# Kernel tuning notes

Hardware: AMD Instinct MI355X
Metric: run time of the kernel (lower is better)

## Reference

```python
import jax, jax.numpy as jnp
import numpy as np

BATCH, T, N, M = 128, 128, 128, 256


def setup_inputs() -> dict:
    key = jax.random.key(0)
    ks = jax.random.split(key, 8)
    s = lambda fan_in: 1.0 / np.sqrt(fan_in)
    return {
        "x": jax.random.normal(ks[0], (BATCH, T, N), dtype=jnp.float32),
        # attention linears (bias=False)
        "We": jax.random.uniform(ks[1], (T, 2 * M), jnp.float32, -s(2 * M), s(2 * M)),
        "Ue": jax.random.uniform(ks[2], (T, T), jnp.float32, -s(T), s(T)),
        "v_e": jax.random.uniform(ks[3], (1, T), jnp.float32, -s(T), s(T)),
        # single-layer LSTM params, PyTorch gate order (i, f, g, o)
        "W_ih": jax.random.uniform(ks[4], (4 * M, N), jnp.float32, -s(M), s(M)),
        "W_hh": jax.random.uniform(ks[5], (4 * M, M), jnp.float32, -s(M), s(M)),
        "b_ih": jax.random.uniform(ks[6], (4 * M,), jnp.float32, -s(M), s(M)),
        "b_hh": jax.random.uniform(ks[7], (4 * M,), jnp.float32, -s(M), s(M)),
    }


def reference(x, We, Ue, v_e, W_ih, W_hh, b_ih, b_hh):
    batch = x.shape[0]
    m = W_hh.shape[1]
    # Ue(x.permute(0,2,1)) is time-invariant: (b, n, T)
    Ux = jnp.einsum("btn,st->bns", x, Ue)
    bias = b_ih + b_hh
    ve = v_e[0]  # (T,)

    def step(carry, x_t):
        h, c = carry  # (b, m) each
        hs = jnp.concatenate([h, c], axis=-1)  # (b, 2m)
        # We(hs) is constant over the feature axis in the original (repeat), so broadcast
        z = jnp.tanh((hs @ We.T)[:, None, :] + Ux)  # (b, n, T)
        scores = jnp.einsum("bnt,t->bn", z, ve)  # v_e linear -> (b, n)
        alpha = jax.nn.softmax(scores, axis=1)  # softmax over features
        xw = x_t * alpha  # (b, n)
        gates = xw @ W_ih.T + h @ W_hh.T + bias  # (b, 4m)
        i, f, g, o = jnp.split(gates, 4, axis=-1)
        c2 = jax.nn.sigmoid(f) * c + jax.nn.sigmoid(i) * jnp.tanh(g)
        h2 = jax.nn.sigmoid(o) * jnp.tanh(c2)
        return (h2, c2), h2

    h0 = jnp.zeros((batch, m), dtype=x.dtype)
    c0 = jnp.zeros((batch, m), dtype=x.dtype)
    xs = jnp.transpose(x, (1, 0, 2))  # (T, b, n)
    _, outs = jax.lax.scan(step, (h0, c0), xs)
    return outs  # (T, b, m)
```

## Files before the change

kernel.cpp:

```cpp
#include <hip/hip_runtime.h>
#include <hip/hip_bf16.h>
#include <hip/hip_fp16.h>

typedef unsigned int uint32;
typedef _Float16 hf2 __attribute__((ext_vector_type(2)));

#define NT 1024

__device__ __forceinline__ float bfu(unsigned short v) { return __uint_as_float(((uint32)v) << 16); }
__device__ __forceinline__ unsigned short f2bf(float f) {
    uint32 u = __float_as_uint(f);
    u = (u + 0x7fffu + ((u >> 16) & 1u)) >> 16;
    return (unsigned short)u;
}
__device__ __forceinline__ uint32 pack_f16(float a, float b) {
    __half ha = __float2half_rn(a), hb = __float2half_rn(b);
    return (uint32)__half_as_ushort(ha) | ((uint32)__half_as_ushort(hb) << 16);
}
__device__ __forceinline__ float fexp2(float x) {
#if __has_builtin(__builtin_amdgcn_exp2f)
    return __builtin_amdgcn_exp2f(x);
#else
    return exp2f(x);
#endif
}
__device__ __forceinline__ float frcp(float x) {
#if __has_builtin(__builtin_amdgcn_rcpf)
    return __builtin_amdgcn_rcpf(x);
#else
    return __fdividef(1.f, x);
#endif
}
__device__ __forceinline__ float fast_tanh(float x) {
    float e = fexp2(x * 2.8853900817779268f);
    return fmaf(-2.f, frcp(1.f + e), 1.f);
}
__device__ __forceinline__ float fast_sigmoid(float x) {
    return frcp(1.f + fexp2(-1.4426950408889634f * x));
}
__device__ __forceinline__ float rdlane(float v, int k) {
#if __has_builtin(__builtin_amdgcn_readlane)
    return __builtin_bit_cast(float, __builtin_amdgcn_readlane(__builtin_bit_cast(int, v), k));
#else
    return __shfl(v, k);
#endif
}
__device__ __forceinline__ float fdot2(uint32 w, uint32 v, float acc) {
#if __has_builtin(__builtin_amdgcn_fdot2)
    return __builtin_amdgcn_fdot2(__builtin_bit_cast(hf2, w), __builtin_bit_cast(hf2, v), acc, false);
#else
    __half2 wh = __builtin_bit_cast(__half2, w), vh = __builtin_bit_cast(__half2, v);
    float2 wf = __half22float2(wh), vf = __half22float2(vh);
    return fmaf(wf.y, vf.y, fmaf(wf.x, vf.x, acc));
#endif
}

template <int S>
__device__ __forceinline__ void spin_ge(uint32* p, uint32 tgt) {
    if (__hip_atomic_load(p, __ATOMIC_ACQUIRE, __HIP_MEMORY_SCOPE_WORKGROUP) >= tgt) return;
    int guard = 0;
    do {
        __builtin_amdgcn_s_sleep(S);
        if (++guard > (1 << 22)) break;
    } while (__hip_atomic_load(p, __ATOMIC_ACQUIRE, __HIP_MEMORY_SCOPE_WORKGROUP) < tgt);
}
__device__ __forceinline__ void st_flag(uint32* p, uint32 v) {
    __hip_atomic_store(p, v, __ATOMIC_RELEASE, __HIP_MEMORY_SCOPE_WORKGROUP);
}
__device__ __forceinline__ void add_flag(uint32* p, uint32 v) {
    __hip_atomic_fetch_add(p, v, __ATOMIC_RELEASE, __HIP_MEMORY_SCOPE_WORKGROUP);
}

__global__ void prep_weights(const float* __restrict__ We, const float* __restrict__ W_ih,
                             const float* __restrict__ W_hh, uint32* __restrict__ We2,
                             uint32* __restrict__ Wc2) {
    int idx = blockIdx.x * 256 + threadIdx.x;
    if (idx < 32768) {
        int p = idx & 3, s = (idx >> 2) & 127, jq = idx >> 9;
        int j = 8 * jq + 2 * p;
        We2[idx] = pack_f16(We[s * 512 + j], We[s * 512 + j + 1]);
    } else if (idx < 229376) {
        int i2 = idx - 32768;
        int p = i2 & 3, q = (i2 >> 2) & 255, np = i2 >> 10;
        int g = 4 * q + p;
        int n0 = 2 * np, n1 = 2 * np + 1;
        float w0, w1;
        if (n0 < 128) {
            w0 = W_ih[g * 128 + n0];
            w1 = W_ih[g * 128 + n1];
        } else {
            w0 = W_hh[g * 256 + (n0 - 128)];
            w1 = W_hh[g * 256 + (n1 - 128)];
        }
        Wc2[i2] = pack_f16(w0, w1);
    }
}

__global__ void ux_kernel(const float* __restrict__ x, const float* __restrict__ Ue,
                          unsigned short* __restrict__ Uxg) {
    int b = blockIdx.x >> 1, h = blockIdx.x & 1;
    int n = threadIdx.x & 127, sg = threadIdx.x >> 7;
    int s0 = h * 64 + sg * 16;
    float acc[16];
#pragma unroll
    for (int k = 0; k < 16; ++k) acc[k] = 0.f;
    for (int t0 = 0; t0 < 128; t0 += 16) {
        float xv[16];
#pragma unroll
        for (int tt = 0; tt < 16; ++tt) xv[tt] = x[(b * 128 + t0 + tt) * 128 + n];
#pragma unroll
        for (int k = 0; k < 16; ++k) {
            const float4* uep = (const float4*)(Ue + (s0 + k) * 128 + t0);
            float4 u0 = uep[0], u1 = uep[1], u2 = uep[2], u3 = uep[3];
            acc[k] += xv[0] * u0.x + xv[1] * u0.y + xv[2] * u0.z + xv[3] * u0.w
                    + xv[4] * u1.x + xv[5] * u1.y + xv[6] * u1.z + xv[7] * u1.w
                    + xv[8] * u2.x + xv[9] * u2.y + xv[10] * u2.z + xv[11] * u2.w
                    + xv[12] * u3.x + xv[13] * u3.y + xv[14] * u3.z + xv[15] * u3.w;
        }
    }
#pragma unroll
    for (int k = 0; k < 16; ++k)
        Uxg[b * 16384 + (s0 + k) * 128 + n] = f2bf(acc[k]);
}

__global__ __launch_bounds__(NT, 4)
void encoder_kernel(const float* __restrict__ x, const float* __restrict__ v_e,
                    const float* __restrict__ b_ih, const float* __restrict__ b_hh,
                    const unsigned short* __restrict__ Uxg, const uint4* __restrict__ We2q,
                    const uint4* __restrict__ Wc2q, float* __restrict__ out) {
    __shared__ __align__(16) unsigned short Ux_s[16384];
    __shared__ __align__(16) uint4 We2L[6144];
    __shared__ __align__(16) float part4[6144];
    __shared__ float part1[256];
    __shared__ float part2[256];
    __shared__ __align__(16) uint32 vh_s[192];
    __shared__ __align__(16) uint32 hsh_s[256];
    __shared__ float c_s[256];
    __shared__ uint32 xw_flag, cnt1, cnt2, cnt4, cnt5;

    const int tid = threadIdx.x;
    const int b = blockIdx.x;

    {
        const uint4* src = (const uint4*)(Uxg + b * 16384);
        uint4* dst = (uint4*)Ux_s;
        for (int i = tid; i < 2048; i += NT) dst[i] = src[i];
    }
    for (int i = tid; i < 6144; i += NT) We2L[i] = We2q[i];
    if (tid < 192) vh_s[tid] = 0u;
    if (tid < 256) { hsh_s[tid] = 0u; c_s[tid] = 0.f; }
    if (tid == 0) { xw_flag = 0; cnt1 = 0; cnt2 = 0; cnt4 = 0; cnt5 = 0; }
    float bi0 = 0.f, bf0 = 0.f, bg0 = 0.f, bo0 = 0.f;
    if (tid >= 768) {
        int j = tid - 768;
        bi0 = b_ih[j] + b_hh[j];
        bf0 = b_ih[256 + j] + b_hh[256 + j];
        bg0 = b_ih[512 + j] + b_hh[512 + j];
        bo0 = b_ih[768 + j] + b_hh[768 + j];
    }
    __syncthreads();

#define NP_BLOCK(npb)                                                \
    {                                                                \
        uint4 vp4 = *(const uint4*)&vh_s[(npb)];                     \
        _Pragma("unroll")                                            \
        for (int u = 0; u < 4; ++u) {                                \
            uint32 vp = (&vp4.x)[u];                                 \
            const uint4* wp = wc + ((npb) + u) * 256;                \
            uint4 w0 = wp[0], w1 = wp[1];                            \
            a0 = fdot2(w0.x, vp, a0); a1 = fdot2(w0.y, vp, a1);      \
            a2 = fdot2(w0.z, vp, a2); a3 = fdot2(w0.w, vp, a3);      \
            a4 = fdot2(w1.x, vp, a4); a5 = fdot2(w1.y, vp, a5);      \
            a6 = fdot2(w1.z, vp, a6); a7 = fdot2(w1.w, vp, a7);      \
        }                                                            \
    }

    if (tid < 768) {
        const int ol = tid & 127, g = tid >> 7;
        if (g >= 4) __builtin_amdgcn_s_setprio(1);
        const uint4* wc = Wc2q + 2 * ol;
        for (int t = 0; t < 128; ++t) {
            float a0 = 0.f, a1 = 0.f, a2 = 0.f, a3 = 0.f;
            float a4 = 0.f, a5 = 0.f, a6 = 0.f, a7 = 0.f;
            if (g < 4) {
                spin_ge<4>(&cnt5, (uint32)(4 * t));
                const int np0 = 64 + g * 32;
#pragma unroll 2
                for (int i = 0; i < 8; ++i) NP_BLOCK(np0 + 4 * i);
            } else {
                spin_ge<1>(&cnt5, (uint32)(4 * t));
                const int s = ol, jg = g - 4;
                float acc = 0.f;
                if (jg == 0) {
#pragma unroll 4
                    for (int jq = 0; jq < 32; ++jq) {
                        uint4 w = We2L[jq * 128 + s];
                        uint4 hh = *(const uint4*)&hsh_s[4 * jq];
                        acc = fdot2(w.x, hh.x, acc);
                        acc = fdot2(w.y, hh.y, acc);
                        acc = fdot2(w.z, hh.z, acc);
                        acc = fdot2(w.w, hh.w, acc);
                    }
                } else {
#pragma unroll 4
                    for (int jq = 32; jq < 48; ++jq) {
                        uint4 w = We2L[jq * 128 + s];
                        uint4 hh = *(const uint4*)&hsh_s[4 * jq];
                        acc = fdot2(w.x, hh.x, acc);
                        acc = fdot2(w.y, hh.y, acc);
                        acc = fdot2(w.z, hh.z, acc);
                        acc = fdot2(w.w, hh.w, acc);
                    }
#pragma unroll 4
                    for (int jq = 48; jq < 64; ++jq) {
                        uint4 w = We2q[jq * 128 + s];
                        uint4 hh = *(const uint4*)&hsh_s[4 * jq];
                        acc = fdot2(w.x, hh.x, acc);
                        acc = fdot2(w.y, hh.y, acc);
                        acc = fdot2(w.z, hh.z, acc);
                        acc = fdot2(w.w, hh.w, acc);
                    }
                }
                part1[jg * 128 + s] = acc;
                if ((tid & 63) == 0) add_flag(&cnt1, 1);
                spin_ge<1>(&xw_flag, (uint32)(t + 1));
                const int np0 = jg * 32;
#pragma unroll 2
                for (int i = 0; i < 8; ++i) NP_BLOCK(np0 + 4 * i);
            }
            float4* p4 = (float4*)&part4[g * 1024 + 8 * ol];
            p4[0] = make_float4(a0, a1, a2, a3);
            p4[1] = make_float4(a4, a5, a6, a7);
            if ((tid & 63) == 0) add_flag(&cnt4, 1);
        }
    } else {
        __builtin_amdgcn_s_setprio(2);
        const int bt = tid - 768, l = tid & 63;
        const int n = bt & 127, sg = bt >> 7;
        const float ve_lane = v_e[sg * 64 + l];
        const unsigned short* uxrow = Ux_s + sg * 64 * 128 + n;
        for (int t = 0; t < 128; ++t) {
            float2 xt2;
            if (bt < 64) xt2 = *(const float2*)(x + (b * 128 + t) * 128 + 2 * l);
            spin_ge<1>(&cnt1, (uint32)(4 * (t + 1)));
            float web_lo = part1[l] + part1[128 + l];
            float web_hi = part1[64 + l] + part1[192 + l];
            float wsel = sg ? web_hi : web_lo;
            float acc0 = 0.f, acc1 = 0.f;
#pragma unroll
            for (int k = 0; k < 64; k += 2) {
                float wv0 = rdlane(wsel, k), ve0 = rdlane(ve_lane, k);
                float wv1 = rdlane(wsel, k + 1), ve1 = rdlane(ve_lane, k + 1);
                acc0 = fmaf(ve0, fast_tanh(wv0 + bfu(uxrow[k * 128])), acc0);
                acc1 = fmaf(ve1, fast_tanh(wv1 + bfu(uxrow[(k + 1) * 128])), acc1);
            }
            part2[sg * 128 + n] = acc0 + acc1;
            if (l == 0) add_flag(&cnt2, 1);
            if (bt < 64) {
                spin_ge<1>(&cnt2, (uint32)(4 * (t + 1)));
                __builtin_amdgcn_s_setprio(3);
                float v0 = part2[2 * l] + part2[128 + 2 * l];
                float v1 = part2[2 * l + 1] + part2[129 + 2 * l];
                float e0 = fexp2(v0 * 1.4426950408889634f);
                float e1 = fexp2(v1 * 1.4426950408889634f);
                float ssum = e0 + e1;
#pragma unroll
                for (int off = 32; off > 0; off >>= 1) ssum += __shfl_xor(ssum, off);
                float inv = frcp(ssum);
                vh_s[l] = pack_f16(xt2.x * e0 * inv, xt2.y * e1 * inv);
                if (bt == 0) st_flag(&xw_flag, (uint32)(t + 1));
                __builtin_amdgcn_s_setprio(2);
            }
            spin_ge<1>(&cnt4, (uint32)(12 * (t + 1)));
            const int j = bt;
            float gi = bi0, gf = bf0, gg = bg0, go = bo0;
#pragma unroll
            for (int gr = 0; gr < 6; ++gr) {
                const float* pp = part4 + gr * 1024;
                gi += pp[j]; gf += pp[256 + j];
                gg += pp[512 + j]; go += pp[768 + j];
            }
            float c = c_s[j];
            float c2 = fast_sigmoid(gf) * c + fast_sigmoid(gi) * fast_tanh(gg);
            float h2v = fast_sigmoid(go) * fast_tanh(c2);
            c_s[j] = c2;
            float hn = __shfl_xor(h2v, 1);
            float cn = __shfl_xor(c2, 1);
            if (!(j & 1)) {
                uint32 hp = pack_f16(h2v, hn);
                vh_s[64 + (j >> 1)] = hp;
                hsh_s[j >> 1] = hp;
                hsh_s[128 + (j >> 1)] = pack_f16(c2, cn);
            }
            if (l == 0) add_flag(&cnt5, 1);
            out[(t * 128 + b) * 256 + j] = h2v;
        }
    }
#undef NP_BLOCK
}

extern "C" void kernel_launch(void* const* d_in, const int* in_sizes, int n_in,
                              void* d_out, int out_size, void* d_ws, size_t ws_size,
                              hipStream_t stream) {
    const float* x    = (const float*)d_in[0];
    const float* We   = (const float*)d_in[1];
    const float* Ue   = (const float*)d_in[2];
    const float* v_e  = (const float*)d_in[3];
    const float* W_ih = (const float*)d_in[4];
    const float* W_hh = (const float*)d_in[5];
    const float* b_ih = (const float*)d_in[6];
    const float* b_hh = (const float*)d_in[7];
    float* out = (float*)d_out;

    char* w = (char*)d_ws;
    unsigned short* Uxg = (unsigned short*)w;
    uint32* We2 = (uint32*)(w + 4194304);
    uint32* Wc2 = (uint32*)(w + 4325376);

    prep_weights<<<896, 256, 0, stream>>>(We, W_ih, W_hh, We2, Wc2);
    ux_kernel<<<256, 512, 0, stream>>>(x, Ue, Uxg);
    encoder_kernel<<<128, NT, 0, stream>>>(x, v_e, b_ih, b_hh, Uxg,
                                           (const uint4*)We2, (const uint4*)Wc2, out);
}
```

Measured before the change: 1.260 ms.

## Defer softmax normalization past xw publish, busy-spin flags, rebalance We partial dot

The softmax-weighted input is published unnormalized, so the x-projection warps can start their dot products before the softmax sum reduction finishes. The reciprocal sum is written to shared memory afterwards and applied to the x-projection partial sums during the gate reduction, at the cost of one extra flag increment (the cnt4 target becomes 13 per step). Spin waits drop s_sleep in favour of pure busy polling to cut wake-up latency, which uses more issue slots while waiting. The We·hs dot product is split evenly between the two warpgroups (24 LDS chunks plus 8 global chunks each) instead of 32 versus 32.

```diff
diff --git a/kernel.cpp b/kernel.cpp
--- a/kernel.cpp
+++ b/kernel.cpp
@@ -63,6 +63,12 @@
         __builtin_amdgcn_s_sleep(S);
         if (++guard > (1 << 22)) break;
     } while (__hip_atomic_load(p, __ATOMIC_ACQUIRE, __HIP_MEMORY_SCOPE_WORKGROUP) < tgt);
+}
+__device__ __forceinline__ void spin_busy(uint32* p, uint32 tgt) {
+    int guard = 0;
+    while (__hip_atomic_load(p, __ATOMIC_ACQUIRE, __HIP_MEMORY_SCOPE_WORKGROUP) < tgt) {
+        if (++guard > (1 << 24)) break;
+    }
 }
 __device__ __forceinline__ void st_flag(uint32* p, uint32 v) {
     __hip_atomic_store(p, v, __ATOMIC_RELEASE, __HIP_MEMORY_SCOPE_WORKGROUP);
@@ -136,6 +142,7 @@
     __shared__ __align__(16) uint32 vh_s[192];
     __shared__ __align__(16) uint32 hsh_s[256];
     __shared__ float c_s[256];
+    __shared__ float inv_s;
     __shared__ uint32 xw_flag, cnt1, cnt2, cnt4, cnt5;
 
     const int tid = threadIdx.x;
@@ -149,7 +156,7 @@
     for (int i = tid; i < 6144; i += NT) We2L[i] = We2q[i];
     if (tid < 192) vh_s[tid] = 0u;
     if (tid < 256) { hsh_s[tid] = 0u; c_s[tid] = 0.f; }
-    if (tid == 0) { xw_flag = 0; cnt1 = 0; cnt2 = 0; cnt4 = 0; cnt5 = 0; }
+    if (tid == 0) { xw_flag = 0; cnt1 = 0; cnt2 = 0; cnt4 = 0; cnt5 = 0; inv_s = 0.f; }
     float bi0 = 0.f, bf0 = 0.f, bg0 = 0.f, bo0 = 0.f;
     if (tid >= 768) {
         int j = tid - 768;
@@ -188,42 +195,32 @@
 #pragma unroll 2
                 for (int i = 0; i < 8; ++i) NP_BLOCK(np0 + 4 * i);
             } else {
-                spin_ge<1>(&cnt5, (uint32)(4 * t));
+                spin_busy(&cnt5, (uint32)(4 * t));
                 const int s = ol, jg = g - 4;
+                const int lq0 = jg * 24;
+                const int gq0 = 48 + jg * 8;
                 float acc = 0.f;
-                if (jg == 0) {
+#pragma unroll
+                for (int jq = gq0; jq < gq0 + 8; ++jq) {
+                    uint4 w = We2q[jq * 128 + s];
+                    uint4 hh = *(const uint4*)&hsh_s[4 * jq];
+                    acc = fdot2(w.x, hh.x, acc);
+                    acc = fdot2(w.y, hh.y, acc);
+                    acc = fdot2(w.z, hh.z, acc);
+                    acc = fdot2(w.w, hh.w, acc);
+                }
 #pragma unroll 4
-                    for (int jq = 0; jq < 32; ++jq) {
-                        uint4 w = We2L[jq * 128 + s];
-                        uint4 hh = *(const uint4*)&hsh_s[4 * jq];
-                        acc = fdot2(w.x, hh.x, acc);
-                        acc = fdot2(w.y, hh.y, acc);
-                        acc = fdot2(w.z, hh.z, acc);
-                        acc = fdot2(w.w, hh.w, acc);
-                    }
-                } else {
-#pragma unroll 4
-                    for (int jq = 32; jq < 48; ++jq) {
-                        uint4 w = We2L[jq * 128 + s];
-                        uint4 hh = *(const uint4*)&hsh_s[4 * jq];
-                        acc = fdot2(w.x, hh.x, acc);
-                        acc = fdot2(w.y, hh.y, acc);
-                        acc = fdot2(w.z, hh.z, acc);
-                        acc = fdot2(w.w, hh.w, acc);
-                    }
-#pragma unroll 4
-                    for (int jq = 48; jq < 64; ++jq) {
-                        uint4 w = We2q[jq * 128 + s];
-                        uint4 hh = *(const uint4*)&hsh_s[4 * jq];
-                        acc = fdot2(w.x, hh.x, acc);
-                        acc = fdot2(w.y, hh.y, acc);
-                        acc = fdot2(w.z, hh.z, acc);
-                        acc = fdot2(w.w, hh.w, acc);
-                    }
+                for (int jq = lq0; jq < lq0 + 24; ++jq) {
+                    uint4 w = We2L[jq * 128 + s];
+                    uint4 hh = *(const uint4*)&hsh_s[4 * jq];
+                    acc = fdot2(w.x, hh.x, acc);
+                    acc = fdot2(w.y, hh.y, acc);
+                    acc = fdot2(w.z, hh.z, acc);
+                    acc = fdot2(w.w, hh.w, acc);
                 }
                 part1[jg * 128 + s] = acc;
                 if ((tid & 63) == 0) add_flag(&cnt1, 1);
-                spin_ge<1>(&xw_flag, (uint32)(t + 1));
+                spin_busy(&xw_flag, (uint32)(t + 1));
                 const int np0 = jg * 32;
 #pragma unroll 2
                 for (int i = 0; i < 8; ++i) NP_BLOCK(np0 + 4 * i);
@@ -242,7 +239,7 @@
         for (int t = 0; t < 128; ++t) {
             float2 xt2;
             if (bt < 64) xt2 = *(const float2*)(x + (b * 128 + t) * 128 + 2 * l);
-            spin_ge<1>(&cnt1, (uint32)(4 * (t + 1)));
+            spin_busy(&cnt1, (uint32)(4 * (t + 1)));
             float web_lo = part1[l] + part1[128 + l];
             float web_hi = part1[64 + l] + part1[192 + l];
             float wsel = sg ? web_hi : web_lo;
@@ -257,29 +254,31 @@
             part2[sg * 128 + n] = acc0 + acc1;
             if (l == 0) add_flag(&cnt2, 1);
             if (bt < 64) {
-                spin_ge<1>(&cnt2, (uint32)(4 * (t + 1)));
+                spin_busy(&cnt2, (uint32)(4 * (t + 1)));
                 __builtin_amdgcn_s_setprio(3);
                 float v0 = part2[2 * l] + part2[128 + 2 * l];
                 float v1 = part2[2 * l + 1] + part2[129 + 2 * l];
                 float e0 = fexp2(v0 * 1.4426950408889634f);
                 float e1 = fexp2(v1 * 1.4426950408889634f);
-                float ssum = e0 + e1;
-#pragma unroll
-                for (int off = 32; off > 0; off >>= 1) ssum += __shfl_xor(ssum, off);
-                float inv = frcp(ssum);
-                vh_s[l] = pack_f16(xt2.x * e0 * inv, xt2.y * e1 * inv);
+                vh_s[l] = pack_f16(xt2.x * e0, xt2.y * e1);
                 if (bt == 0) st_flag(&xw_flag, (uint32)(t + 1));
                 __builtin_amdgcn_s_setprio(2);
+                float ssum = e0 + e1;
+#pragma unroll
+                for (int off = 32; off > 0; off >>= 1) ssum += __shfl_xor(ssum, off);
+                if (bt == 0) { inv_s = frcp(ssum); add_flag(&cnt4, 1); }
             }
-            spin_ge<1>(&cnt4, (uint32)(12 * (t + 1)));
+            spin_busy(&cnt4, (uint32)(13 * (t + 1)));
+            const float inv = inv_s;
             const int j = bt;
-            float gi = bi0, gf = bf0, gg = bg0, go = bo0;
-#pragma unroll
-            for (int gr = 0; gr < 6; ++gr) {
-                const float* pp = part4 + gr * 1024;
-                gi += pp[j]; gf += pp[256 + j];
-                gg += pp[512 + j]; go += pp[768 + j];
-            }
+            float gi = bi0 + part4[j] + part4[1024 + j] + part4[2048 + j] + part4[3072 + j]
+                     + (part4[4096 + j] + part4[5120 + j]) * inv;
+            float gf = bf0 + part4[256 + j] + part4[1280 + j] + part4[2304 + j] + part4[3328 + j]
+                     + (part4[4352 + j] + part4[5376 + j]) * inv;
+            float gg = bg0 + part4[512 + j] + part4[1536 + j] + part4[2560 + j] + part4[3584 + j]
+                     + (part4[4608 + j] + part4[5632 + j]) * inv;
+            float go = bo0 + part4[768 + j] + part4[1792 + j] + part4[2816 + j] + part4[3840 + j]
+                     + (part4[4864 + j] + part4[5888 + j]) * inv;
             float c = c_s[j];
             float c2 = fast_sigmoid(gf) * c + fast_sigmoid(gi) * fast_tanh(gg);
             float h2v = fast_sigmoid(go) * fast_tanh(c2);
```

New measurement: 1.055 ms (median of 2 runs). 1.19x faster.
